# Kernel tuning notes

Measured on AMD Instinct MI355X. Metric: run time of the kernel, lower is better.

The kernel has to match this reference:

```python
import jax, jax.numpy as jnp
import numpy as np

N, D, H, O, E = 50000, 512, 512, 256, 150000
NEG_SLOPE = 0.2
EPS = 1e-16


def gat_conv(x, edge_index, W_src, W_dst, a_src, a_dst, bias):
    """Single-head PyG GATConv, add_self_loops=False.
    x: [N, Din]; edge_index: [2, E] (row 0 = src, row 1 = dst).
    W_src/W_dst: [Din, C]; a_src/a_dst: [C]; bias: [C].
    """
    src, dst = edge_index[0], edge_index[1]
    h_src = x @ W_src                      # [N, C]
    h_dst = x @ W_dst                      # [N, C]
    alpha_src = h_src @ a_src              # [N]
    alpha_dst = h_dst @ a_dst              # [N]
    e = jax.nn.leaky_relu(alpha_src[src] + alpha_dst[dst], NEG_SLOPE)  # [E]
    # per-destination segment softmax (numerically stable)
    m = jax.ops.segment_max(e, dst, num_segments=N)       # [N]
    ex = jnp.exp(e - m[dst])                               # [E]
    s = jax.ops.segment_sum(ex, dst, num_segments=N)       # [N]
    alpha = ex / (s[dst] + EPS)                            # [E]
    # scatter-add weighted source messages to destinations
    out = jax.ops.segment_sum(alpha[:, None] * h_src[src], dst, num_segments=N)  # [N, C]
    return out + bias


def setup_inputs() -> dict:
    key = jax.random.key(0)
    ks = jax.random.split(key, 20)
    g = lambda i, shape, sc: (jax.random.normal(ks[i], shape, dtype=jnp.float32) * sc)
    inp = {
        "x": jax.random.normal(ks[0], (N, D), dtype=jnp.float32),
        "edge_index": jax.random.randint(ks[1], (2, E), 0, N, dtype=jnp.int32),
        "edge_index_2_hop": jax.random.randint(ks[2], (2, E), 0, N, dtype=jnp.int32),
        # conv1 (D -> H)
        "W1_src": g(3, (D, H), 0.05), "W1_dst": g(4, (D, H), 0.05),
        "a1_src": g(5, (H,), 0.05), "a1_dst": g(6, (H,), 0.05),
        "b1": jnp.zeros((H,), jnp.float32),
        # lin1 (H -> H)
        "Wl1": g(7, (H, H), 0.05), "bl1": jnp.zeros((H,), jnp.float32),
        # conv2 (H -> O)
        "W2_src": g(8, (H, O), 0.05), "W2_dst": g(9, (H, O), 0.05),
        "a2_src": g(10, (O,), 0.05), "a2_dst": g(11, (O,), 0.05),
        "b2": jnp.zeros((O,), jnp.float32),
        # lin2 (O -> O)
        "Wl2": g(12, (O, O), 0.05), "bl2": jnp.zeros((O,), jnp.float32),
    }
    return inp


def reference(x, edge_index, edge_index_2_hop,
              W1_src, W1_dst, a1_src, a1_dst, b1, Wl1, bl1,
              W2_src, W2_dst, a2_src, a2_dst, b2, Wl2, bl2):
    h = (gat_conv(x, edge_index, W1_src, W1_dst, a1_src, a1_dst, b1)
         + gat_conv(x, edge_index_2_hop, W1_src, W1_dst, a1_src, a1_dst, b1))
    h = jax.nn.relu(h @ Wl1 + bl1)
    h = (gat_conv(h, edge_index, W2_src, W2_dst, a2_src, a2_dst, b2)
         + gat_conv(h, edge_index_2_hop, W2_src, W2_dst, a2_src, a2_dst, b2))
    return h @ Wl2 + bl2
```

## Files before the change

### kernel.cpp

```cpp
#include <hip/hip_runtime.h>

typedef unsigned short u16;
typedef __attribute__((ext_vector_type(8))) unsigned short v8u16;
typedef __attribute__((ext_vector_type(4))) unsigned short v4u16;
typedef __attribute__((ext_vector_type(8))) __bf16 v8bf;
typedef __attribute__((ext_vector_type(4))) float v4f;

#define NN 50000
#define EE 150000
#define SCAN_CHUNK 512
#define NB_PER_SET 98

__device__ inline float b2f(u16 u) {
    union { unsigned int i; float f; } x; x.i = ((unsigned int)u) << 16; return x.f;
}
__device__ inline u16 f2b(float f) {
    union { float f; unsigned int i; } x; x.f = f;
    unsigned int r = x.i + 0x7FFFu + ((x.i >> 16) & 1u);
    return (u16)(r >> 16);
}
__device__ inline float wred(float v) {
    v += __shfl_down(v, 32, 64);
    v += __shfl_down(v, 16, 64);
    v += __shfl_down(v, 8, 64);
    v += __shfl_down(v, 4, 64);
    v += __shfl_down(v, 2, 64);
    v += __shfl_down(v, 1, 64);
    return v;
}
__device__ inline int wred_i(int v) {
    v += __shfl_down(v, 32, 64);
    v += __shfl_down(v, 16, 64);
    v += __shfl_down(v, 8, 64);
    v += __shfl_down(v, 4, 64);
    v += __shfl_down(v, 2, 64);
    v += __shfl_down(v, 1, 64);
    return v;
}

__device__ __forceinline__ void gll16(const u16* g, u16* l) {
    __builtin_amdgcn_global_load_lds(
        (const __attribute__((address_space(1))) void*)g,
        (__attribute__((address_space(3))) void*)l, 16, 0, 0);
}


__global__ void transpose4(const float* __restrict__ W0, u16* __restrict__ T0,
                           const float* __restrict__ W1, u16* __restrict__ T1,
                           const float* __restrict__ W2, u16* __restrict__ T2,
                           const float* __restrict__ W3, u16* __restrict__ T3) {
    int idx = blockIdx.x * blockDim.x + threadIdx.x;
    const float* W; u16* T; int N, K, base;
    if (idx < 262144)      { W = W0; T = T0; K = 512; N = 512; base = 0; }
    else if (idx < 524288) { W = W1; T = T1; K = 512; N = 512; base = 262144; }
    else if (idx < 655360) { W = W2; T = T2; K = 512; N = 256; base = 524288; }
    else if (idx < 720896) { W = W3; T = T3; K = 256; N = 256; base = 655360; }
    else return;
    int i = idx - base;
    int n = i % N, k = i / N;
    T[(size_t)n * K + k] = f2b(W[i]);
}

__global__ void wv4(const float* __restrict__ Wa, const float* __restrict__ Wb,
                    const float* __restrict__ Wc, const float* __restrict__ Wd,
                    const float* __restrict__ aa, const float* __restrict__ ab,
                    const float* __restrict__ ac, const float* __restrict__ ad,
                    float* __restrict__ vbuf) {
    int rw = (blockIdx.x * blockDim.x + threadIdx.x) >> 6;
    int lane = threadIdx.x & 63;
    if (rw >= 2048) return;
    int seg = rw >> 9, r = rw & 511;
    const float* W; const float* a; int C;
    if (seg == 0)      { W = Wa; a = aa; C = 512; }
    else if (seg == 1) { W = Wb; a = ab; C = 512; }
    else if (seg == 2) { W = Wc; a = ac; C = 256; }
    else               { W = Wd; a = ad; C = 256; }
    float s = 0.f;
    int c0 = lane * 8;
    if (c0 < C) {
        const float* wp = W + (size_t)r * C + c0;
        v4f w0 = *(const v4f*)wp;
        v4f w1 = *(const v4f*)(wp + 4);
        v4f a0 = *(const v4f*)(a + c0);
        v4f a1 = *(const v4f*)(a + c0 + 4);
#pragma unroll
        for (int j = 0; j < 4; ++j) s += w0[j] * a0[j] + w1[j] * a1[j];
    }
    s = wred(s);
    if (lane == 0) vbuf[rw] = s;
}

__global__ void alpha_pair_f32x(const float* __restrict__ X, const float* __restrict__ vs,
                                const float* __restrict__ vd, float* __restrict__ as_,
                                float* __restrict__ ad_, u16* __restrict__ Xb, int Nn) {
    int w = (blockIdx.x * blockDim.x + threadIdx.x) >> 6;
    int lane = threadIdx.x & 63;
    if (w >= Nn) return;
    const float* xp = X + (size_t)w * 512 + lane * 8;
    v4f x0 = *(const v4f*)xp;
    v4f x1 = *(const v4f*)(xp + 4);
    const float* vsp = vs + lane * 8;
    const float* vdp = vd + lane * 8;
    float s1 = 0.f, s2 = 0.f;
    v8u16 o;
#pragma unroll
    for (int j = 0; j < 4; ++j) {
        s1 += x0[j] * vsp[j] + x1[j] * vsp[j + 4];
        s2 += x0[j] * vdp[j] + x1[j] * vdp[j + 4];
        o[j] = f2b(x0[j]); o[j + 4] = f2b(x1[j]);
    }
    *(v8u16*)(Xb + (size_t)w * 512 + lane * 8) = o;
    s1 = wred(s1);
    s2 = wred(s2);
    if (lane == 0) { as_[w] = s1; ad_[w] = s2; }
}


__global__ void deg2_kernel(const int* __restrict__ ei1, const int* __restrict__ ei2,
                            int* __restrict__ deg) {
    int idx = blockIdx.x * blockDim.x + threadIdx.x;
    if (idx >= 2 * EE) return;
    int set = idx >= EE;
    int e = idx - set * EE;
    const int* ei = set ? ei2 : ei1;
    atomicAdd(&deg[set * NN + ei[EE + e]], 1);
}

__global__ void scan_partial(const int* __restrict__ deg, int* __restrict__ bsum) {
    int b = blockIdx.x;
    int set = b / NB_PER_SET, lb = b - set * NB_PER_SET;
    int tid = threadIdx.x;
    int i0 = lb * SCAN_CHUNK + tid * 2;
    int s = 0;
    if (i0 < NN)     s += deg[set * NN + i0];
    if (i0 + 1 < NN) s += deg[set * NN + i0 + 1];
    s = wred_i(s);
    __shared__ int lsum[4];
    if ((tid & 63) == 0) lsum[tid >> 6] = s;
    __syncthreads();
    if (tid == 0) bsum[b] = lsum[0] + lsum[1] + lsum[2] + lsum[3];
}

__global__ void scan_tops(int* __restrict__ bsum) {
    __shared__ int ls[256];
    int tid = threadIdx.x;
    int set = tid >> 7, lb = tid & 127;
    int v = (lb < NB_PER_SET) ? bsum[set * NB_PER_SET + lb] : 0;
    ls[tid] = v;
    __syncthreads();
    for (int off = 1; off < 128; off <<= 1) {
        int t = (lb >= off) ? ls[tid - off] : 0;
        __syncthreads();
        ls[tid] += t;
        __syncthreads();
    }
    if (lb < NB_PER_SET) bsum[set * NB_PER_SET + lb] = ls[tid] - v;
}

__global__ void scan_final(const int* __restrict__ deg, const int* __restrict__ bsum,
                           int* __restrict__ rp) {
    int b = blockIdx.x;
    int set = b / NB_PER_SET, lb = b - set * NB_PER_SET;
    int tid = threadIdx.x;
    int i0 = lb * SCAN_CHUNK + tid * 2;
    int d0 = (i0 < NN)     ? deg[set * NN + i0]     : 0;
    int d1 = (i0 + 1 < NN) ? deg[set * NN + i0 + 1] : 0;
    int pair = d0 + d1;
    __shared__ int ps[256];
    ps[tid] = pair;
    __syncthreads();
    for (int off = 1; off < 256; off <<= 1) {
        int t = (tid >= off) ? ps[tid - off] : 0;
        __syncthreads();
        ps[tid] += t;
        __syncthreads();
    }
    int base = bsum[b] + ps[tid] - pair;
    if (i0 < NN)     rp[set * (NN + 1) + i0] = base;
    if (i0 + 1 < NN) rp[set * (NN + 1) + i0 + 1] = base + d0;
    if (b == 0 && tid == 0) { rp[NN] = EE; rp[(NN + 1) + NN] = EE; }
}

__global__ void fill2_kernel(const int* __restrict__ ei1, const int* __restrict__ ei2,
                             const int* __restrict__ rp, int* __restrict__ deg,
                             int* __restrict__ srcp, int* __restrict__ dstp) {
    int idx = blockIdx.x * blockDim.x + threadIdx.x;
    if (idx >= 2 * EE) return;
    int set = idx >= EE;
    int e = idx - set * EE;
    const int* ei = set ? ei2 : ei1;
    int d = ei[EE + e];
    int old = atomicSub(&deg[set * NN + d], 1);
    int pos = rp[set * (NN + 1) + d] + old - 1;
    srcp[set * EE + pos] = ei[e];
    dstp[set * EE + pos] = d;
}

__global__ void edge_ex(const int* __restrict__ srcp, const int* __restrict__ dstp,
                        const float* __restrict__ asrc, const float* __restrict__ adst,
                        float* __restrict__ ex) {
    int i = blockIdx.x * blockDim.x + threadIdx.x;
    if (i >= 2 * EE) return;
    float t = asrc[srcp[i]] + adst[dstp[i]];
    t = t > 0.f ? t : 0.2f * t;
    ex[i] = __expf(fminf(t, 60.f));
}

template <int CV>
__global__ void gat_pull(const int* __restrict__ rp, const int* __restrict__ srcp,
                         const float* __restrict__ ex, const u16* __restrict__ H,
                         const float* __restrict__ bias, u16* __restrict__ G, int Nn) {
    const int C = CV * 64;
    int d = (blockIdx.x * blockDim.x + threadIdx.x) >> 6;
    int lane = threadIdx.x & 63;
    if (d >= Nn) return;
    float out[CV];
#pragma unroll
    for (int j = 0; j < CV; ++j) out[j] = 0.f;
#pragma unroll
    for (int set = 0; set < 2; ++set) {
        const int* rpS = rp + set * (NN + 1);
        int base = set * EE;
        int beg = rpS[d], end = rpS[d + 1];
        float acc[CV];
#pragma unroll
        for (int j = 0; j < CV; ++j) acc[j] = 0.f;
        float ssum = 0.f;
        if (beg < end) {
            float w0 = ex[base + beg];
            int s0 = srcp[base + beg];
            if constexpr (CV == 8) {
                v8u16 h0 = *(const v8u16*)(H + (size_t)s0 * C + lane * 8);
                for (int i = beg + 1; i < end; ++i) {
                    float w1 = ex[base + i];
                    int s1 = srcp[base + i];
                    v8u16 h1 = *(const v8u16*)(H + (size_t)s1 * C + lane * 8);
                    ssum += w0;
#pragma unroll
                    for (int j = 0; j < 8; ++j) acc[j] += w0 * b2f(h0[j]);
                    w0 = w1; h0 = h1;
                }
                ssum += w0;
#pragma unroll
                for (int j = 0; j < 8; ++j) acc[j] += w0 * b2f(h0[j]);
            } else {
                v4u16 h0 = *(const v4u16*)(H + (size_t)s0 * C + lane * 4);
                for (int i = beg + 1; i < end; ++i) {
                    float w1 = ex[base + i];
                    int s1 = srcp[base + i];
                    v4u16 h1 = *(const v4u16*)(H + (size_t)s1 * C + lane * 4);
                    ssum += w0;
#pragma unroll
                    for (int j = 0; j < 4; ++j) acc[j] += w0 * b2f(h0[j]);
                    w0 = w1; h0 = h1;
                }
                ssum += w0;
#pragma unroll
                for (int j = 0; j < 4; ++j) acc[j] += w0 * b2f(h0[j]);
            }
        }
        float inv = 1.f / (ssum + 1e-16f);
#pragma unroll
        for (int j = 0; j < CV; ++j) out[j] += acc[j] * inv;
    }
    const float* bp = bias + lane * CV;
    u16* gp = G + (size_t)d * C + lane * CV;
    if constexpr (CV == 8) {
        v8u16 o;
#pragma unroll
        for (int j = 0; j < 8; ++j) o[j] = f2b(out[j] + 2.f * bp[j]);
        *(v8u16*)gp = o;
    } else {
        v4u16 o;
#pragma unroll
        for (int j = 0; j < 4; ++j) o[j] = f2b(out[j] + 2.f * bp[j]);
        *(v4u16*)gp = o;
    }
}

__global__ __launch_bounds__(256, 2) void gemm_bf16(
    const u16* __restrict__ A, const u16* __restrict__ Bt, void* __restrict__ Cv,
    int M, int N, int K, const float* __restrict__ bias, int relu, int outf32,
    const float* __restrict__ avs, const float* __restrict__ avd,
    float* __restrict__ aout_s, float* __restrict__ aout_d) {
    __shared__ u16 As[128 * 32];
    __shared__ u16 Bs[128 * 32];
    const int tid = threadIdx.x;
    const int lane = tid & 63;
    const int wid = tid >> 6;
    const int wm = wid >> 1;
    const int wn = wid & 1;
    const int quad = lane >> 4;
    const int l16 = lane & 15;

    const int nwg = gridDim.x * gridDim.y;
    const int orig = blockIdx.y * gridDim.x + blockIdx.x;
    const int q = nwg >> 3, r = nwg & 7;
    const int xcd = orig & 7, loc = orig >> 3;
    const int wg = (xcd < r ? xcd * (q + 1) : r * (q + 1) + (xcd - r) * q) + loc;
    const int tileM = (wg / gridDim.x) * 128;
    const int tileN = (wg % gridDim.x) * 128;

    const int srow = tid >> 2;
    const int scol = (tid & 3) * 8;
    int ra0 = tileM + srow;       if (ra0 >= M) ra0 = M - 1;
    int ra1 = tileM + 64 + srow;  if (ra1 >= M) ra1 = M - 1;
    const u16* gA0 = A + (size_t)ra0 * K + scol;
    const u16* gA1 = A + (size_t)ra1 * K + scol;
    const u16* gB0 = Bt + (size_t)(tileN + srow) * K + scol;
    const u16* gB1 = Bt + (size_t)(tileN + 64 + srow) * K + scol;
    u16* lA0 = As + wid * 512;
    u16* lA1 = As + 2048 + wid * 512;
    u16* lB0 = Bs + wid * 512;
    u16* lB1 = Bs + 2048 + wid * 512;

    v4f acc[4][4];
#pragma unroll
    for (int i = 0; i < 4; ++i)
#pragma unroll
        for (int j = 0; j < 4; ++j) acc[i][j] = v4f{0.f, 0.f, 0.f, 0.f};

    for (int k0 = 0; k0 < K; k0 += 32) {
        gll16(gA0 + k0, lA0);
        gll16(gA1 + k0, lA1);
        gll16(gB0 + k0, lB0);
        gll16(gB1 + k0, lB1);
        __syncthreads();
        v8bf af[4], bfr[4];
#pragma unroll
        for (int i = 0; i < 4; ++i)
            af[i] = __builtin_bit_cast(v8bf, *(const v8u16*)&As[(wm * 64 + i * 16 + l16) * 32 + quad * 8]);
#pragma unroll
        for (int i = 0; i < 4; ++i)
            bfr[i] = __builtin_bit_cast(v8bf, *(const v8u16*)&Bs[(wn * 64 + i * 16 + l16) * 32 + quad * 8]);
#pragma unroll
        for (int mi = 0; mi < 4; ++mi)
#pragma unroll
            for (int ni = 0; ni < 4; ++ni)
                acc[mi][ni] = __builtin_amdgcn_mfma_f32_16x16x32_bf16(af[mi], bfr[ni], acc[mi][ni], 0, 0, 0);
        __syncthreads();
    }

    float rs[4][4], rd[4][4];
#pragma unroll
    for (int mi = 0; mi < 4; ++mi)
#pragma unroll
        for (int rr = 0; rr < 4; ++rr) { rs[mi][rr] = 0.f; rd[mi][rr] = 0.f; }

#pragma unroll
    for (int mi = 0; mi < 4; ++mi)
#pragma unroll
        for (int ni = 0; ni < 4; ++ni) {
            int col = tileN + wn * 64 + ni * 16 + l16;
            float bb = bias ? bias[col] : 0.f;
            float ws_ = avs ? avs[col] : 0.f;
            float wd_ = avd ? avd[col] : 0.f;
            int row0 = tileM + wm * 64 + mi * 16 + quad * 4;
#pragma unroll
            for (int rr = 0; rr < 4; ++rr) {
                int row = row0 + rr;
                if (row < M) {
                    float v = acc[mi][ni][rr] + bb;
                    if (relu) v = fmaxf(v, 0.f);
                    if (outf32) ((float*)Cv)[(size_t)row * N + col] = v;
                    else        ((u16*)Cv)[(size_t)row * N + col] = f2b(v);
                    rs[mi][rr] += v * ws_;
                    rd[mi][rr] += v * wd_;
                }
            }
        }

    if (avs) {
#pragma unroll
        for (int mi = 0; mi < 4; ++mi)
#pragma unroll
            for (int rr = 0; rr < 4; ++rr) {
                int row = tileM + wm * 64 + mi * 16 + quad * 4 + rr;
                float a = rs[mi][rr], b = rd[mi][rr];
                a += __shfl_down(a, 8, 64); a += __shfl_down(a, 4, 64);
                a += __shfl_down(a, 2, 64); a += __shfl_down(a, 1, 64);
                b += __shfl_down(b, 8, 64); b += __shfl_down(b, 4, 64);
                b += __shfl_down(b, 2, 64); b += __shfl_down(b, 1, 64);
                if (l16 == 0 && row < M) {
                    atomicAdd(&aout_s[row], a);
                    atomicAdd(&aout_d[row], b);
                }
            }
    }
}


extern "C" void kernel_launch(void* const* d_in, const int* in_sizes, int n_in,
                              void* d_out, int out_size, void* d_ws, size_t ws_size,
                              hipStream_t stream) {
    const float* x  = (const float*)d_in[0];
    const int* ei1  = (const int*)d_in[1];
    const int* ei2  = (const int*)d_in[2];
    const float* W1s = (const float*)d_in[3];
    const float* W1d = (const float*)d_in[4];
    const float* a1s = (const float*)d_in[5];
    const float* a1d = (const float*)d_in[6];
    const float* b1  = (const float*)d_in[7];
    const float* Wl1 = (const float*)d_in[8];
    const float* bl1 = (const float*)d_in[9];
    const float* W2s = (const float*)d_in[10];
    const float* W2d = (const float*)d_in[11];
    const float* a2s = (const float*)d_in[12];
    const float* a2d = (const float*)d_in[13];
    const float* b2  = (const float*)d_in[14];
    const float* Wl2 = (const float*)d_in[15];
    const float* bl2 = (const float*)d_in[16];
    float* out = (float*)d_out;

    char* ws = (char*)d_ws;
    size_t off = 0;
    auto alloc = [&](size_t b) { void* p = ws + off; off = (off + b + 255) & ~(size_t)255; return p; };
    u16* bufA   = (u16*)alloc((size_t)NN * 512 * 2);
    u16* bufB   = (u16*)alloc((size_t)NN * 512 * 2);
    int* rp     = (int*)alloc((size_t)2 * (NN + 1) * 4);
    int* srcp   = (int*)alloc((size_t)2 * EE * 4);
    int* dstp   = (int*)alloc((size_t)2 * EE * 4);
    int* deg    = (int*)alloc((size_t)2 * NN * 4);
    int* bsum   = (int*)alloc((size_t)2 * NB_PER_SET * 4);
    float* ex   = (float*)alloc((size_t)2 * EE * 4);
    float* asrc = (float*)alloc((size_t)NN * 4);
    float* adst = (float*)alloc((size_t)NN * 4);
    float* vbuf = (float*)alloc(2048 * 4);
    u16* Wt1s   = (u16*)alloc((size_t)512 * 512 * 2);
    u16* Wtl1   = (u16*)alloc((size_t)512 * 512 * 2);
    u16* Wt2s   = (u16*)alloc((size_t)512 * 256 * 2);
    u16* Wtl2   = (u16*)alloc((size_t)256 * 256 * 2);
    u16* g2buf  = bufB + (size_t)NN * 256;

    hipMemsetAsync(deg, 0, (size_t)2 * NN * 4, stream);
    deg2_kernel<<<(2 * EE + 255) / 256, 256, 0, stream>>>(ei1, ei2, deg);
    scan_partial<<<2 * NB_PER_SET, 256, 0, stream>>>(deg, bsum);
    scan_tops<<<1, 256, 0, stream>>>(bsum);
    scan_final<<<2 * NB_PER_SET, 256, 0, stream>>>(deg, bsum, rp);
    fill2_kernel<<<(2 * EE + 255) / 256, 256, 0, stream>>>(ei1, ei2, rp, deg, srcp, dstp);

    transpose4<<<(720896 + 255) / 256, 256, 0, stream>>>(W1s, Wt1s, Wl1, Wtl1, W2s, Wt2s, Wl2, Wtl2);
    wv4<<<512, 256, 0, stream>>>(W1s, W1d, W2s, W2d, a1s, a1d, a2s, a2d, vbuf);

    alpha_pair_f32x<<<(NN + 3) / 4, 256, 0, stream>>>(x, vbuf, vbuf + 512, asrc, adst, bufB, NN);
    edge_ex<<<(2 * EE + 255) / 256, 256, 0, stream>>>(srcp, dstp, asrc, adst, ex);
    gemm_bf16<<<dim3(4, 391), 256, 0, stream>>>(bufB, Wt1s, bufA, NN, 512, 512, nullptr, 0, 0,
                                                nullptr, nullptr, nullptr, nullptr);
    gat_pull<8><<<(NN + 3) / 4, 256, 0, stream>>>(rp, srcp, ex, bufA, b1, bufB, NN);
    hipMemsetAsync(asrc, 0, (size_t)NN * 4, stream);
    hipMemsetAsync(adst, 0, (size_t)NN * 4, stream);
    gemm_bf16<<<dim3(4, 391), 256, 0, stream>>>(bufB, Wtl1, bufA, NN, 512, 512, bl1, 1, 0,
                                                vbuf + 1024, vbuf + 1536, asrc, adst);

    edge_ex<<<(2 * EE + 255) / 256, 256, 0, stream>>>(srcp, dstp, asrc, adst, ex);
    gemm_bf16<<<dim3(2, 391), 256, 0, stream>>>(bufA, Wt2s, bufB, NN, 256, 512, nullptr, 0, 0,
                                                nullptr, nullptr, nullptr, nullptr);
    gat_pull<4><<<(NN + 3) / 4, 256, 0, stream>>>(rp, srcp, ex, bufB, b2, g2buf, NN);
    gemm_bf16<<<dim3(2, 391), 256, 0, stream>>>(g2buf, Wtl2, out, NN, 256, 256, bl2, 0, 1,
                                                nullptr, nullptr, nullptr, nullptr);

    (void)in_sizes; (void)n_in; (void)out_size; (void)ws_size;
}
```

Measured before the change: 507.7 us.

## Fuse edge score into gat_pull, drop dstp/ex, tile transpose, split GEMMs

```diff
diff --git a/kernel.cpp b/kernel.cpp
--- a/kernel.cpp
+++ b/kernel.cpp
@@ -45,20 +45,33 @@
 }
 
 
-__global__ void transpose4(const float* __restrict__ W0, u16* __restrict__ T0,
-                           const float* __restrict__ W1, u16* __restrict__ T1,
-                           const float* __restrict__ W2, u16* __restrict__ T2,
-                           const float* __restrict__ W3, u16* __restrict__ T3) {
-    int idx = blockIdx.x * blockDim.x + threadIdx.x;
-    const float* W; u16* T; int N, K, base;
-    if (idx < 262144)      { W = W0; T = T0; K = 512; N = 512; base = 0; }
-    else if (idx < 524288) { W = W1; T = T1; K = 512; N = 512; base = 262144; }
-    else if (idx < 655360) { W = W2; T = T2; K = 512; N = 256; base = 524288; }
-    else if (idx < 720896) { W = W3; T = T3; K = 256; N = 256; base = 655360; }
-    else return;
-    int i = idx - base;
-    int n = i % N, k = i / N;
-    T[(size_t)n * K + k] = f2b(W[i]);
+__global__ void transpose4t(const float* __restrict__ W0, u16* __restrict__ T0,
+                            const float* __restrict__ W1, u16* __restrict__ T1,
+                            const float* __restrict__ W2, u16* __restrict__ T2,
+                            const float* __restrict__ W3, u16* __restrict__ T3) {
+    int b = blockIdx.x;
+    const float* W; u16* T; int N, K, t;
+    if (b < 256)      { W = W0; T = T0; K = 512; N = 512; t = b; }
+    else if (b < 512) { W = W1; T = T1; K = 512; N = 512; t = b - 256; }
+    else if (b < 640) { W = W2; T = T2; K = 512; N = 256; t = b - 512; }
+    else              { W = W3; T = T3; K = 256; N = 256; t = b - 640; }
+    const int tilesN = N >> 5;
+    const int kb = (t / tilesN) << 5;
+    const int nb = (t % tilesN) << 5;
+    __shared__ u16 tile[32][33];
+    const int c = threadIdx.x & 31;
+    const int r0 = threadIdx.x >> 5;
+#pragma unroll
+    for (int rr = 0; rr < 4; ++rr) {
+        int r = r0 + rr * 8;
+        tile[r][c] = f2b(W[(size_t)(kb + r) * N + nb + c]);
+    }
+    __syncthreads();
+#pragma unroll
+    for (int rr = 0; rr < 4; ++rr) {
+        int r = r0 + rr * 8;
+        T[(size_t)(nb + r) * K + kb + c] = tile[c][r];
+    }
 }
 
 __global__ void wv4(const float* __restrict__ Wa, const float* __restrict__ Wb,
@@ -183,7 +196,7 @@
 
 __global__ void fill2_kernel(const int* __restrict__ ei1, const int* __restrict__ ei2,
                              const int* __restrict__ rp, int* __restrict__ deg,
-                             int* __restrict__ srcp, int* __restrict__ dstp) {
+                             int* __restrict__ srcp) {
     int idx = blockIdx.x * blockDim.x + threadIdx.x;
     if (idx >= 2 * EE) return;
     int set = idx >= EE;
@@ -193,70 +206,100 @@
     int old = atomicSub(&deg[set * NN + d], 1);
     int pos = rp[set * (NN + 1) + d] + old - 1;
     srcp[set * EE + pos] = ei[e];
-    dstp[set * EE + pos] = d;
-}
-
-__global__ void edge_ex(const int* __restrict__ srcp, const int* __restrict__ dstp,
-                        const float* __restrict__ asrc, const float* __restrict__ adst,
-                        float* __restrict__ ex) {
-    int i = blockIdx.x * blockDim.x + threadIdx.x;
-    if (i >= 2 * EE) return;
-    float t = asrc[srcp[i]] + adst[dstp[i]];
-    t = t > 0.f ? t : 0.2f * t;
-    ex[i] = __expf(fminf(t, 60.f));
 }
 
 template <int CV>
 __global__ void gat_pull(const int* __restrict__ rp, const int* __restrict__ srcp,
-                         const float* __restrict__ ex, const u16* __restrict__ H,
-                         const float* __restrict__ bias, u16* __restrict__ G, int Nn) {
+                         const float* __restrict__ asrc, const float* __restrict__ adst,
+                         const u16* __restrict__ H, const float* __restrict__ bias,
+                         u16* __restrict__ G, int Nn) {
     const int C = CV * 64;
     int d = (blockIdx.x * blockDim.x + threadIdx.x) >> 6;
     int lane = threadIdx.x & 63;
     if (d >= Nn) return;
+    const float ad = adst[d];
     float out[CV];
 #pragma unroll
     for (int j = 0; j < CV; ++j) out[j] = 0.f;
 #pragma unroll
     for (int set = 0; set < 2; ++set) {
         const int* rpS = rp + set * (NN + 1);
-        int base = set * EE;
+        const int* srcS = srcp + set * EE;
         int beg = rpS[d], end = rpS[d + 1];
         float acc[CV];
 #pragma unroll
         for (int j = 0; j < CV; ++j) acc[j] = 0.f;
         float ssum = 0.f;
-        if (beg < end) {
-            float w0 = ex[base + beg];
-            int s0 = srcp[base + beg];
+        int n = end - beg;
+        if (n > 0) {
             if constexpr (CV == 8) {
+                int s0 = srcS[beg];
+                float a0 = asrc[s0];
                 v8u16 h0 = *(const v8u16*)(H + (size_t)s0 * C + lane * 8);
-                for (int i = beg + 1; i < end; ++i) {
-                    float w1 = ex[base + i];
-                    int s1 = srcp[base + i];
-                    v8u16 h1 = *(const v8u16*)(H + (size_t)s1 * C + lane * 8);
-                    ssum += w0;
-#pragma unroll
-                    for (int j = 0; j < 8; ++j) acc[j] += w0 * b2f(h0[j]);
-                    w0 = w1; h0 = h1;
-                }
-                ssum += w0;
-#pragma unroll
-                for (int j = 0; j < 8; ++j) acc[j] += w0 * b2f(h0[j]);
+                float a1 = 0.f; v8u16 h1{};
+                if (n > 1) {
+                    int s1 = srcS[beg + 1];
+                    a1 = asrc[s1];
+                    h1 = *(const v8u16*)(H + (size_t)s1 * C + lane * 8);
+                }
+                for (int i = beg + 2; i < end; ++i) {
+                    int s2 = srcS[i];
+                    float a2 = asrc[s2];
+                    v8u16 h2 = *(const v8u16*)(H + (size_t)s2 * C + lane * 8);
+                    float t = a0 + ad; t = t > 0.f ? t : 0.2f * t;
+                    float w = __expf(fminf(t, 60.f));
+                    ssum += w;
+#pragma unroll
+                    for (int j = 0; j < 8; ++j) acc[j] += w * b2f(h0[j]);
+                    a0 = a1; h0 = h1; a1 = a2; h1 = h2;
+                }
+                if (n > 1) {
+                    float t = a0 + ad; t = t > 0.f ? t : 0.2f * t;
+                    float w = __expf(fminf(t, 60.f));
+                    ssum += w;
+#pragma unroll
+                    for (int j = 0; j < 8; ++j) acc[j] += w * b2f(h0[j]);
+                    a0 = a1; h0 = h1;
+                }
+                float t = a0 + ad; t = t > 0.f ? t : 0.2f * t;
+                float w = __expf(fminf(t, 60.f));
+                ssum += w;
+#pragma unroll
+                for (int j = 0; j < 8; ++j) acc[j] += w * b2f(h0[j]);
             } else {
+                int s0 = srcS[beg];
+                float a0 = asrc[s0];
                 v4u16 h0 = *(const v4u16*)(H + (size_t)s0 * C + lane * 4);
-                for (int i = beg + 1; i < end; ++i) {
-                    float w1 = ex[base + i];
-                    int s1 = srcp[base + i];
-                    v4u16 h1 = *(const v4u16*)(H + (size_t)s1 * C + lane * 4);
-                    ssum += w0;
-#pragma unroll
-                    for (int j = 0; j < 4; ++j) acc[j] += w0 * b2f(h0[j]);
-                    w0 = w1; h0 = h1;
-                }
-                ssum += w0;
-#pragma unroll
-                for (int j = 0; j < 4; ++j) acc[j] += w0 * b2f(h0[j]);
+                float a1 = 0.f; v4u16 h1{};
+                if (n > 1) {
+                    int s1 = srcS[beg + 1];
+                    a1 = asrc[s1];
+                    h1 = *(const v4u16*)(H + (size_t)s1 * C + lane * 4);
+                }
+                for (int i = beg + 2; i < end; ++i) {
+                    int s2 = srcS[i];
+                    float a2 = asrc[s2];
+                    v4u16 h2 = *(const v4u16*)(H + (size_t)s2 * C + lane * 4);
+                    float t = a0 + ad; t = t > 0.f ? t : 0.2f * t;
+                    float w = __expf(fminf(t, 60.f));
+                    ssum += w;
+#pragma unroll
+                    for (int j = 0; j < 4; ++j) acc[j] += w * b2f(h0[j]);
+                    a0 = a1; h0 = h1; a1 = a2; h1 = h2;
+                }
+                if (n > 1) {
+                    float t = a0 + ad; t = t > 0.f ? t : 0.2f * t;
+                    float w = __expf(fminf(t, 60.f));
+                    ssum += w;
+#pragma unroll
+                    for (int j = 0; j < 4; ++j) acc[j] += w * b2f(h0[j]);
+                    a0 = a1; h0 = h1;
+                }
+                float t = a0 + ad; t = t > 0.f ? t : 0.2f * t;
+                float w = __expf(fminf(t, 60.f));
+                ssum += w;
+#pragma unroll
+                for (int j = 0; j < 4; ++j) acc[j] += w * b2f(h0[j]);
             }
         }
         float inv = 1.f / (ssum + 1e-16f);
@@ -292,14 +335,8 @@
     const int wn = wid & 1;
     const int quad = lane >> 4;
     const int l16 = lane & 15;
-
-    const int nwg = gridDim.x * gridDim.y;
-    const int orig = blockIdx.y * gridDim.x + blockIdx.x;
-    const int q = nwg >> 3, r = nwg & 7;
-    const int xcd = orig & 7, loc = orig >> 3;
-    const int wg = (xcd < r ? xcd * (q + 1) : r * (q + 1) + (xcd - r) * q) + loc;
-    const int tileM = (wg / gridDim.x) * 128;
-    const int tileN = (wg % gridDim.x) * 128;
+    const int tileM = blockIdx.y * 128;
+    const int tileN = blockIdx.x * 128;
 
     const int srow = tid >> 2;
     const int scol = (tid & 3) * 8;
@@ -419,10 +456,11 @@
     u16* bufB   = (u16*)alloc((size_t)NN * 512 * 2);
     int* rp     = (int*)alloc((size_t)2 * (NN + 1) * 4);
     int* srcp   = (int*)alloc((size_t)2 * EE * 4);
-    int* dstp   = (int*)alloc((size_t)2 * EE * 4);
-    int* deg    = (int*)alloc((size_t)2 * NN * 4);
+    int* zblk   = (int*)alloc((size_t)4 * NN * 4);
+    int* deg    = zblk;
+    float* asrc2 = (float*)(zblk + 2 * NN);
+    float* adst2 = (float*)(zblk + 3 * NN);
     int* bsum   = (int*)alloc((size_t)2 * NB_PER_SET * 4);
-    float* ex   = (float*)alloc((size_t)2 * EE * 4);
     float* asrc = (float*)alloc((size_t)NN * 4);
     float* adst = (float*)alloc((size_t)NN * 4);
     float* vbuf = (float*)alloc(2048 * 4);
@@ -432,30 +470,37 @@
     u16* Wtl2   = (u16*)alloc((size_t)256 * 256 * 2);
     u16* g2buf  = bufB + (size_t)NN * 256;
 
-    hipMemsetAsync(deg, 0, (size_t)2 * NN * 4, stream);
+    const int MH0 = 25088;
+    const int MH1 = NN - MH0;
+
+    hipMemsetAsync(zblk, 0, (size_t)4 * NN * 4, stream);
     deg2_kernel<<<(2 * EE + 255) / 256, 256, 0, stream>>>(ei1, ei2, deg);
     scan_partial<<<2 * NB_PER_SET, 256, 0, stream>>>(deg, bsum);
     scan_tops<<<1, 256, 0, stream>>>(bsum);
     scan_final<<<2 * NB_PER_SET, 256, 0, stream>>>(deg, bsum, rp);
-    fill2_kernel<<<(2 * EE + 255) / 256, 256, 0, stream>>>(ei1, ei2, rp, deg, srcp, dstp);
-
-    transpose4<<<(720896 + 255) / 256, 256, 0, stream>>>(W1s, Wt1s, Wl1, Wtl1, W2s, Wt2s, Wl2, Wtl2);
+    fill2_kernel<<<(2 * EE + 255) / 256, 256, 0, stream>>>(ei1, ei2, rp, deg, srcp);
+
+    transpose4t<<<704, 256, 0, stream>>>(W1s, Wt1s, Wl1, Wtl1, W2s, Wt2s, Wl2, Wtl2);
     wv4<<<512, 256, 0, stream>>>(W1s, W1d, W2s, W2d, a1s, a1d, a2s, a2d, vbuf);
 
+    auto gemm2x = [&](const u16* A, const u16* Bt, void* Cv, int N, int K,
+                      const float* bias, int relu, int outf32,
+                      const float* avs, const float* avd, float* as_, float* ad_) {
+        gemm_bf16<<<dim3(N / 128, MH0 / 128), 256, 0, stream>>>(
+            A, Bt, Cv, MH0, N, K, bias, relu, outf32, avs, avd, as_, ad_);
+        gemm_bf16<<<dim3(N / 128, (MH1 + 127) / 128), 256, 0, stream>>>(
+            A + (size_t)MH0 * K, Bt, (char*)Cv + (size_t)MH0 * N * (outf32 ? 4 : 2),
+            MH1, N, K, bias, relu, outf32, avs, avd,
+            as_ ? as_ + MH0 : nullptr, ad_ ? ad_ + MH0 : nullptr);
+    };
+
     alpha_pair_f32x<<<(NN + 3) / 4, 256, 0, stream>>>(x, vbuf, vbuf + 512, asrc, adst, bufB, NN);
-    edge_ex<<<(2 * EE + 255) / 256, 256, 0, stream>>>(srcp, dstp, asrc, adst, ex);
-    gemm_bf16<<<dim3(4, 391), 256, 0, stream>>>(bufB, Wt1s, bufA, NN, 512, 512, nullptr, 0, 0,
-                                                nullptr, nullptr, nullptr, nullptr);
-    gat_pull<8><<<(NN + 3) / 4, 256, 0, stream>>>(rp, srcp, ex, bufA, b1, bufB, NN);
-    hipMemsetAsync(asrc, 0, (size_t)NN * 4, stream);
-    hipMemsetAsync(adst, 0, (size_t)NN * 4, stream);
-    gemm_bf16<<<dim3(4, 391), 256, 0, stream>>>(bufB, Wtl1, bufA, NN, 512, 512, bl1, 1, 0,
-                                                vbuf + 1024, vbuf + 1536, asrc, adst);
-
-    edge_ex<<<(2 * EE + 255) / 256, 256, 0, stream>>>(srcp, dstp, asrc, adst, ex);
-    gemm_bf16<<<dim3(2, 391), 256, 0, stream>>>(bufA, Wt2s, bufB, NN, 256, 512, nullptr, 0, 0,
-                                                nullptr, nullptr, nullptr, nullptr);
-    gat_pull<4><<<(NN + 3) / 4, 256, 0, stream>>>(rp, srcp, ex, bufB, b2, g2buf, NN);
+    gemm2x(bufB, Wt1s, bufA, 512, 512, nullptr, 0, 0, nullptr, nullptr, nullptr, nullptr);
+    gat_pull<8><<<(NN + 3) / 4, 256, 0, stream>>>(rp, srcp, asrc, adst, bufA, b1, bufB, NN);
+    gemm2x(bufB, Wtl1, bufA, 512, 512, bl1, 1, 0, vbuf + 1024, vbuf + 1536, asrc2, adst2);
+
+    gemm2x(bufA, Wt2s, bufB, 256, 512, nullptr, 0, 0, nullptr, nullptr, nullptr, nullptr);
+    gat_pull<4><<<(NN + 3) / 4, 256, 0, stream>>>(rp, srcp, asrc2, adst2, bufB, b2, g2buf, NN);
     gemm_bf16<<<dim3(2, 391), 256, 0, stream>>>(g2buf, Wtl2, out, NN, 256, 256, bl2, 0, 1,
                                                 nullptr, nullptr, nullptr, nullptr);
 
```

New measurement: 550.1 us. 1.08x slower.
